# Kernel tuning notes

Hardware: AMD Instinct MI355X
Metric: run time of the kernel (lower is better)

The kernel has to match this reference:

```python
import jax, jax.numpy as jnp
import numpy as np

B = 128
E, IN, H, OUT, ZD = 6, 1664, 512, 618, 32


def setup_inputs() -> dict:
    key = jax.random.key(0)
    ks = jax.random.split(key, 9)
    scale = 0.05
    return {
        "p_prev": jax.random.normal(ks[0], (B, IN), dtype=jnp.float32),
        "blending_coef": jax.random.uniform(ks[1], (B, E), dtype=jnp.float32),
        "z": jax.random.normal(ks[2], (B, ZD), dtype=jnp.float32),
        "w_l1": jax.random.normal(ks[3], (E, IN, H), dtype=jnp.float32) * scale,
        "b_l1": jax.random.normal(ks[4], (E, H), dtype=jnp.float32) * scale,
        "w_l2": jax.random.normal(ks[5], (E, H + ZD, H), dtype=jnp.float32) * scale,
        "b_l2": jax.random.normal(ks[6], (E, H + ZD, H)[0:0] + (E, H), dtype=jnp.float32) * scale,
        "w_l3": jax.random.normal(ks[7], (E, H + ZD, OUT), dtype=jnp.float32) * scale,
        "b_l3": jax.random.normal(ks[8], (E, OUT), dtype=jnp.float32) * scale,
    }


def _moe_layer(x, coef, w, b, use_act=True):
    # Per-sample blended weight matmul, fused as a single contraction:
    # y[b,o] = sum_i x[b,i] * (sum_e coef[b,e] * w[e,i,o]) + sum_e coef[b,e] * b[e,o]
    y = jnp.einsum("bi,eio,be->bo", x, w, coef) + jnp.einsum("be,eo->bo", coef, b)
    return jax.nn.elu(y) if use_act else y


def reference(p_prev, blending_coef, z, w_l1, b_l1, w_l2, b_l2, w_l3, b_l3):
    x = _moe_layer(p_prev, blending_coef, w_l1, b_l1)              # [B, H]
    x = _moe_layer(jnp.concatenate([x, z], axis=-1), blending_coef, w_l2, b_l2)  # [B, H]
    x = _moe_layer(jnp.concatenate([x, z], axis=-1), blending_coef, w_l3, b_l3, use_act=False)  # [B, OUT]
    return x
```

## Files before the change

### kernel.cpp

```cpp
#include <hip/hip_runtime.h>
#include <math.h>

#define B 128
#define E 6
#define IN_DIM 1664
#define H_DIM 512
#define OUT_DIM 618
#define ZD 32
#define K2 544

typedef __attribute__((ext_vector_type(8))) short short8;
typedef __attribute__((ext_vector_type(4))) float f32x4;
union U128 { uint4 u4; short8 s8; ushort us[8]; };

__device__ __forceinline__ ushort f2bf(float f) {
    uint u = __float_as_uint(f);
    u += 0x7fffu + ((u >> 16) & 1u);
    return (ushort)(u >> 16);
}
__device__ __forceinline__ uint pk2(float a, float b) {
    return (uint)f2bf(a) | ((uint)f2bf(b) << 16);
}
__device__ __forceinline__ float elu1(float x) { return x < 0.f ? expm1f(x) : x; }


__global__ __launch_bounds__(256) void init_y1(
    const float* __restrict__ coef, const float* __restrict__ b1,
    float* __restrict__ y1)
{
    const int t = blockIdx.x * 256 + threadIdx.x;
    const int b = t >> 7, o = (t & 127) << 2;
    float4 v = {0.f, 0.f, 0.f, 0.f};
    #pragma unroll
    for (int e = 0; e < E; ++e) {
        const float c = coef[b * E + e];
        const float4 bb = *reinterpret_cast<const float4*>(b1 + e * H_DIM + o);
        v.x = fmaf(c, bb.x, v.x); v.y = fmaf(c, bb.y, v.y);
        v.z = fmaf(c, bb.z, v.z); v.w = fmaf(c, bb.w, v.w);
    }
    *reinterpret_cast<float4*>(y1 + b * H_DIM + o) = v;
}

__global__ __launch_bounds__(256) void gemm1(
    const float* __restrict__ x,
    const float* __restrict__ coef,
    const float* __restrict__ w,
    const float* __restrict__ b2, const float* __restrict__ b3,
    float* __restrict__ y1, float* __restrict__ y2, float* __restrict__ out)
{
    __shared__ ushort bs[24][64][8];
    const int tid = threadIdx.x;

    if (blockIdx.y == 0) {
        const int t = blockIdx.x * 256 + tid;
        {
            const int b = t >> 7, o = (t & 127) << 2;
            float4 v = {0.f, 0.f, 0.f, 0.f};
            #pragma unroll
            for (int e = 0; e < E; ++e) {
                const float c = coef[b * E + e];
                const float4 bb = *reinterpret_cast<const float4*>(b2 + e * H_DIM + o);
                v.x = fmaf(c, bb.x, v.x); v.y = fmaf(c, bb.y, v.y);
                v.z = fmaf(c, bb.z, v.z); v.w = fmaf(c, bb.w, v.w);
            }
            *reinterpret_cast<float4*>(y2 + b * H_DIM + o) = v;
        }
        for (int i = t; i < B * OUT_DIM; i += 64 * 256) {
            const int b = i / OUT_DIM, o = i - b * OUT_DIM;
            float v = 0.f;
            #pragma unroll
            for (int e = 0; e < E; ++e)
                v = fmaf(coef[b * E + e], b3[e * OUT_DIM + o], v);
            out[i] = v;
        }
        return;
    }

    const int kb0 = (blockIdx.y - 1) * 4;
    const int n0 = (blockIdx.x & 31) * 16, rowbase = (blockIdx.x >> 5) * 64;
    const int l = tid & 63, wv = tid >> 6;
    const int tn = tid & 15, tq = tid >> 4;
    const int lp = ((tq >> 2) << 4) | tn, j0 = (2 * tq) & 7;
    const int row = rowbase + wv * 16 + (l & 15);
    const int kq = l >> 4;

    float ce[E];
    #pragma unroll
    for (int e = 0; e < E; ++e) ce[e] = coef[row * E + e];

    float xv[4][8];
    #pragma unroll
    for (int kbi = 0; kbi < 4; ++kbi) {
        const float* p = x + (size_t)row * IN_DIM + (kb0 + kbi) * 32 + kq * 8;
        const float4 a = *reinterpret_cast<const float4*>(p);
        const float4 b = *reinterpret_cast<const float4*>(p + 4);
        xv[kbi][0] = a.x; xv[kbi][1] = a.y; xv[kbi][2] = a.z; xv[kbi][3] = a.w;
        xv[kbi][4] = b.x; xv[kbi][5] = b.y; xv[kbi][6] = b.z; xv[kbi][7] = b.w;
    }

    #pragma unroll
    for (int bb = 0; bb < 2; ++bb) {
        float wr[12][2];
        #pragma unroll
        for (int ss = 0; ss < 12; ++ss) {
            const int s = bb * 12 + ss;
            const int e = s % E, kb = kb0 + s / E;
            const float* src = w + ((size_t)e * IN_DIM + kb * 32 + 2 * tq) * H_DIM + n0 + tn;
            wr[ss][0] = src[0];
            wr[ss][1] = src[H_DIM];
        }
        #pragma unroll
        for (int ss = 0; ss < 12; ++ss)
            *reinterpret_cast<uint*>(&bs[bb * 12 + ss][lp][j0]) =
                pk2(wr[ss][0], wr[ss][1]);
    }
    __syncthreads();

    f32x4 acc = {0.f, 0.f, 0.f, 0.f};
    #pragma unroll
    for (int s = 0; s < 24; ++s) {
        const int e = s % E, kbi = s / E;
        U128 a, b0;
        #pragma unroll
        for (int j = 0; j < 8; ++j) a.us[j] = f2bf(xv[kbi][j] * ce[e]);
        b0.u4 = *reinterpret_cast<const uint4*>(&bs[s][l][0]);
        acc = __builtin_amdgcn_mfma_f32_16x16x32_bf16(a.s8, b0.s8, acc, 0, 0, 0);
    }

    const int colB = n0 + (l & 15);
    const int rowE = rowbase + wv * 16 + ((l >> 4) << 2);
    #pragma unroll
    for (int r = 0; r < 4; ++r)
        atomicAdd(&y1[(size_t)(rowE + r) * H_DIM + colB], acc[r]);
}

template<int KPB, bool ZS, int NW, bool GUARD>
__device__ __forceinline__ void gemm_mid_body(
    const float* __restrict__ yin,
    const float* __restrict__ coef,
    const float* __restrict__ z,
    const float* __restrict__ w,
    float* __restrict__ yout,
    int n0, int rowbase, int kb0, ushort (*bs)[64][8])
{
    constexpr int NS = E * KPB;
    const int tid = threadIdx.x;
    const int l = tid & 63, wv = tid >> 6;
    const int tn = tid & 15, tq = tid >> 4;
    const int lp = ((tq >> 2) << 4) | tn, j0 = (2 * tq) & 7;
    const int row = rowbase + wv * 16 + (l & 15);
    const int kq = l >> 4;
    const bool okS = !GUARD || (n0 + tn) < NW;

    float wr[NS][2];
    #pragma unroll
    for (int s = 0; s < NS; ++s) {
        const int e = s % E, kb = kb0 + s / E;
        const float* src = w + ((size_t)e * K2 + kb * 32 + 2 * tq) * NW + n0 + tn;
        wr[s][0] = okS ? src[0] : 0.f;
        wr[s][1] = okS ? src[NW] : 0.f;
    }

    float ce[E];
    #pragma unroll
    for (int e = 0; e < E; ++e) ce[e] = coef[row * E + e];

    float v[KPB * 8];
    if (ZS) {
        const float4 a = *reinterpret_cast<const float4*>(z + row * ZD + kq * 8);
        const float4 b = *reinterpret_cast<const float4*>(z + row * ZD + kq * 8 + 4);
        v[0] = a.x; v[1] = a.y; v[2] = a.z; v[3] = a.w;
        v[4] = b.x; v[5] = b.y; v[6] = b.z; v[7] = b.w;
    } else {
        #pragma unroll
        for (int kbi = 0; kbi < KPB; ++kbi) {
            const float* p = yin + (size_t)row * H_DIM + (kb0 + kbi) * 32 + kq * 8;
            const float4 a = *reinterpret_cast<const float4*>(p);
            const float4 b = *reinterpret_cast<const float4*>(p + 4);
            v[kbi*8+0] = elu1(a.x); v[kbi*8+1] = elu1(a.y);
            v[kbi*8+2] = elu1(a.z); v[kbi*8+3] = elu1(a.w);
            v[kbi*8+4] = elu1(b.x); v[kbi*8+5] = elu1(b.y);
            v[kbi*8+6] = elu1(b.z); v[kbi*8+7] = elu1(b.w);
        }
    }

    #pragma unroll
    for (int s = 0; s < NS; ++s)
        *reinterpret_cast<uint*>(&bs[s][lp][j0]) = pk2(wr[s][0], wr[s][1]);
    __syncthreads();

    f32x4 acc = {0.f, 0.f, 0.f, 0.f};
    #pragma unroll
    for (int s = 0; s < NS; ++s) {
        const int e = s % E, kbi = s / E;
        U128 a, b0;
        #pragma unroll
        for (int j = 0; j < 8; ++j) a.us[j] = f2bf(v[kbi * 8 + j] * ce[e]);
        b0.u4 = *reinterpret_cast<const uint4*>(&bs[s][l][0]);
        acc = __builtin_amdgcn_mfma_f32_16x16x32_bf16(a.s8, b0.s8, acc, 0, 0, 0);
    }

    const int colB = n0 + (l & 15);
    const int rowE = rowbase + wv * 16 + ((l >> 4) << 2);
    if (!GUARD || colB < NW) {
        #pragma unroll
        for (int r = 0; r < 4; ++r)
            atomicAdd(&yout[(size_t)(rowE + r) * NW + colB], acc[r]);
    }
}

__global__ __launch_bounds__(256) void gemm_l2(
    const float* __restrict__ y1, const float* __restrict__ coef,
    const float* __restrict__ z, const float* __restrict__ w2,
    float* __restrict__ y2)
{
    __shared__ ushort bs[12][64][8];
    const int n0 = (blockIdx.x & 31) * 16, rowbase = (blockIdx.x >> 5) * 64;
    const int sp = blockIdx.y;
    if (sp < 8)
        gemm_mid_body<2, false, H_DIM, false>(y1, coef, z, w2, y2,
                                              n0, rowbase, sp * 2, bs);
    else
        gemm_mid_body<1, true, H_DIM, false>(y1, coef, z, w2, y2,
                                             n0, rowbase, 16, bs);
}

__global__ __launch_bounds__(256) void gemm_l3(
    const float* __restrict__ y2, const float* __restrict__ coef,
    const float* __restrict__ z, const float* __restrict__ w3,
    float* __restrict__ out)
{
    __shared__ ushort bs[12][64][8];
    const int nt = blockIdx.x % 40, rt = blockIdx.x / 40;
    const int n0 = nt * 16, rowbase = rt * 64;
    const int sp = blockIdx.y;
    if (sp < 8)
        gemm_mid_body<2, false, OUT_DIM, true>(y2, coef, z, w3, out,
                                               n0, rowbase, sp * 2, bs);
    else
        gemm_mid_body<1, true, OUT_DIM, true>(y2, coef, z, w3, out,
                                              n0, rowbase, 16, bs);
}

extern "C" void kernel_launch(void* const* d_in, const int* in_sizes, int n_in,
                              void* d_out, int out_size, void* d_ws, size_t ws_size,
                              hipStream_t stream)
{
    const float* p_prev = (const float*)d_in[0];
    const float* coef   = (const float*)d_in[1];
    const float* z      = (const float*)d_in[2];
    const float* w1     = (const float*)d_in[3];
    const float* b1     = (const float*)d_in[4];
    const float* w2     = (const float*)d_in[5];
    const float* b2     = (const float*)d_in[6];
    const float* w3     = (const float*)d_in[7];
    const float* b3     = (const float*)d_in[8];
    float* out = (float*)d_out;

    float* y1 = (float*)d_ws;
    float* y2 = y1 + (size_t)B * H_DIM;

    init_y1<<<64, 256, 0, stream>>>(coef, b1, y1);
    gemm1<<<dim3(64, 14), 256, 0, stream>>>(p_prev, coef, w1, b2, b3,
                                            y1, y2, out);
    gemm_l2<<<dim3(64, 9), 256, 0, stream>>>(y1, coef, z, w2, y2);
    gemm_l3<<<dim3(80, 9), 256, 0, stream>>>(y2, coef, z, w3, out);
}
```

Before: 41.46 us.

## Apply blending coefficients after MFMA via per-expert accumulators

Instead of scaling the activation row by each expert coefficient and converting to bf16 before every MFMA, activations are converted to bf16 once and reused for all experts. Six separate accumulators are kept per expert, and the coefficients are applied in fp32 in the epilogue before the atomic add. The bf16 conversion also switches to the HIP intrinsic. This removes many per-step multiply and convert instructions from the MFMA loop, at the cost of more accumulator registers and a slightly different rounding order.

Result: slower. 43.98 us (+6.1%).

```diff
diff --git a/kernel.cpp b/kernel.cpp
--- a/kernel.cpp
+++ b/kernel.cpp
@@ -1,4 +1,5 @@
 #include <hip/hip_runtime.h>
+#include <hip/hip_bf16.h>
 #include <math.h>
 
 #define B 128
@@ -13,13 +14,11 @@
 typedef __attribute__((ext_vector_type(4))) float f32x4;
 union U128 { uint4 u4; short8 s8; ushort us[8]; };
 
-__device__ __forceinline__ ushort f2bf(float f) {
-    uint u = __float_as_uint(f);
-    u += 0x7fffu + ((u >> 16) & 1u);
-    return (ushort)(u >> 16);
-}
 __device__ __forceinline__ uint pk2(float a, float b) {
-    return (uint)f2bf(a) | ((uint)f2bf(b) << 16);
+    union { __hip_bfloat162 h2; uint u; } cv;
+    cv.h2.x = __float2bfloat16(a);
+    cv.h2.y = __float2bfloat16(b);
+    return cv.u;
 }
 __device__ __forceinline__ float elu1(float x) { return x < 0.f ? expm1f(x) : x; }
 
@@ -81,21 +80,26 @@
     const int l = tid & 63, wv = tid >> 6;
     const int tn = tid & 15, tq = tid >> 4;
     const int lp = ((tq >> 2) << 4) | tn, j0 = (2 * tq) & 7;
-    const int row = rowbase + wv * 16 + (l & 15);
+    const int rowA = rowbase + wv * 16 + (l & 15);
+    const int rowE = rowbase + wv * 16 + ((l >> 4) << 2);
     const int kq = l >> 4;
 
-    float ce[E];
-    #pragma unroll
-    for (int e = 0; e < E; ++e) ce[e] = coef[row * E + e];
-
-    float xv[4][8];
+    float cf[4][E];
+    #pragma unroll
+    for (int r = 0; r < 4; ++r)
+        #pragma unroll
+        for (int e = 0; e < E; ++e)
+            cf[r][e] = coef[(rowE + r) * E + e];
+
+    U128 ax[4];
     #pragma unroll
     for (int kbi = 0; kbi < 4; ++kbi) {
-        const float* p = x + (size_t)row * IN_DIM + (kb0 + kbi) * 32 + kq * 8;
+        const float* p = x + (size_t)rowA * IN_DIM + (kb0 + kbi) * 32 + kq * 8;
         const float4 a = *reinterpret_cast<const float4*>(p);
         const float4 b = *reinterpret_cast<const float4*>(p + 4);
-        xv[kbi][0] = a.x; xv[kbi][1] = a.y; xv[kbi][2] = a.z; xv[kbi][3] = a.w;
-        xv[kbi][4] = b.x; xv[kbi][5] = b.y; xv[kbi][6] = b.z; xv[kbi][7] = b.w;
+        uint* au = reinterpret_cast<uint*>(&ax[kbi]);
+        au[0] = pk2(a.x, a.y); au[1] = pk2(a.z, a.w);
+        au[2] = pk2(b.x, b.y); au[3] = pk2(b.z, b.w);
     }
 
     #pragma unroll
@@ -116,22 +120,26 @@
     }
     __syncthreads();
 
-    f32x4 acc = {0.f, 0.f, 0.f, 0.f};
+    f32x4 acc[E];
+    #pragma unroll
+    for (int e = 0; e < E; ++e) acc[e] = {0.f, 0.f, 0.f, 0.f};
     #pragma unroll
     for (int s = 0; s < 24; ++s) {
         const int e = s % E, kbi = s / E;
-        U128 a, b0;
-        #pragma unroll
-        for (int j = 0; j < 8; ++j) a.us[j] = f2bf(xv[kbi][j] * ce[e]);
+        U128 b0;
         b0.u4 = *reinterpret_cast<const uint4*>(&bs[s][l][0]);
-        acc = __builtin_amdgcn_mfma_f32_16x16x32_bf16(a.s8, b0.s8, acc, 0, 0, 0);
+        acc[e] = __builtin_amdgcn_mfma_f32_16x16x32_bf16(ax[kbi].s8, b0.s8,
+                                                         acc[e], 0, 0, 0);
     }
 
     const int colB = n0 + (l & 15);
-    const int rowE = rowbase + wv * 16 + ((l >> 4) << 2);
-    #pragma unroll
-    for (int r = 0; r < 4; ++r)
-        atomicAdd(&y1[(size_t)(rowE + r) * H_DIM + colB], acc[r]);
+    #pragma unroll
+    for (int r = 0; r < 4; ++r) {
+        float val = 0.f;
+        #pragma unroll
+        for (int e = 0; e < E; ++e) val = fmaf(cf[r][e], acc[e][r], val);
+        atomicAdd(&y1[(size_t)(rowE + r) * H_DIM + colB], val);
+    }
 }
 
 template<int KPB, bool ZS, int NW, bool GUARD>
@@ -148,7 +156,8 @@
     const int l = tid & 63, wv = tid >> 6;
     const int tn = tid & 15, tq = tid >> 4;
     const int lp = ((tq >> 2) << 4) | tn, j0 = (2 * tq) & 7;
-    const int row = rowbase + wv * 16 + (l & 15);
+    const int rowA = rowbase + wv * 16 + (l & 15);
+    const int rowE = rowbase + wv * 16 + ((l >> 4) << 2);
     const int kq = l >> 4;
     const bool okS = !GUARD || (n0 + tn) < NW;
 
@@ -161,26 +170,30 @@
         wr[s][1] = okS ? src[NW] : 0.f;
     }
 
-    float ce[E];
-    #pragma unroll
-    for (int e = 0; e < E; ++e) ce[e] = coef[row * E + e];
-
-    float v[KPB * 8];
+    float cf[4][E];
+    #pragma unroll
+    for (int r = 0; r < 4; ++r)
+        #pragma unroll
+        for (int e = 0; e < E; ++e)
+            cf[r][e] = coef[(rowE + r) * E + e];
+
+    U128 ax[KPB];
     if (ZS) {
-        const float4 a = *reinterpret_cast<const float4*>(z + row * ZD + kq * 8);
-        const float4 b = *reinterpret_cast<const float4*>(z + row * ZD + kq * 8 + 4);
-        v[0] = a.x; v[1] = a.y; v[2] = a.z; v[3] = a.w;
-        v[4] = b.x; v[5] = b.y; v[6] = b.z; v[7] = b.w;
+        const float* p = z + rowA * ZD + kq * 8;
+        const float4 a = *reinterpret_cast<const float4*>(p);
+        const float4 b = *reinterpret_cast<const float4*>(p + 4);
+        uint* au = reinterpret_cast<uint*>(&ax[0]);
+        au[0] = pk2(a.x, a.y); au[1] = pk2(a.z, a.w);
+        au[2] = pk2(b.x, b.y); au[3] = pk2(b.z, b.w);
     } else {
         #pragma unroll
         for (int kbi = 0; kbi < KPB; ++kbi) {
-            const float* p = yin + (size_t)row * H_DIM + (kb0 + kbi) * 32 + kq * 8;
+            const float* p = yin + (size_t)rowA * H_DIM + (kb0 + kbi) * 32 + kq * 8;
             const float4 a = *reinterpret_cast<const float4*>(p);
             const float4 b = *reinterpret_cast<const float4*>(p + 4);
-            v[kbi*8+0] = elu1(a.x); v[kbi*8+1] = elu1(a.y);
-            v[kbi*8+2] = elu1(a.z); v[kbi*8+3] = elu1(a.w);
-            v[kbi*8+4] = elu1(b.x); v[kbi*8+5] = elu1(b.y);
-            v[kbi*8+6] = elu1(b.z); v[kbi*8+7] = elu1(b.w);
+            uint* au = reinterpret_cast<uint*>(&ax[kbi]);
+            au[0] = pk2(elu1(a.x), elu1(a.y)); au[1] = pk2(elu1(a.z), elu1(a.w));
+            au[2] = pk2(elu1(b.x), elu1(b.y)); au[3] = pk2(elu1(b.z), elu1(b.w));
         }
     }
 
@@ -189,23 +202,27 @@
         *reinterpret_cast<uint*>(&bs[s][lp][j0]) = pk2(wr[s][0], wr[s][1]);
     __syncthreads();
 
-    f32x4 acc = {0.f, 0.f, 0.f, 0.f};
+    f32x4 acc[E];
+    #pragma unroll
+    for (int e = 0; e < E; ++e) acc[e] = {0.f, 0.f, 0.f, 0.f};
     #pragma unroll
     for (int s = 0; s < NS; ++s) {
         const int e = s % E, kbi = s / E;
-        U128 a, b0;
-        #pragma unroll
-        for (int j = 0; j < 8; ++j) a.us[j] = f2bf(v[kbi * 8 + j] * ce[e]);
+        U128 b0;
         b0.u4 = *reinterpret_cast<const uint4*>(&bs[s][l][0]);
-        acc = __builtin_amdgcn_mfma_f32_16x16x32_bf16(a.s8, b0.s8, acc, 0, 0, 0);
+        acc[e] = __builtin_amdgcn_mfma_f32_16x16x32_bf16(ax[kbi].s8, b0.s8,
+                                                         acc[e], 0, 0, 0);
     }
 
     const int colB = n0 + (l & 15);
-    const int rowE = rowbase + wv * 16 + ((l >> 4) << 2);
     if (!GUARD || colB < NW) {
         #pragma unroll
-        for (int r = 0; r < 4; ++r)
-            atomicAdd(&yout[(size_t)(rowE + r) * NW + colB], acc[r]);
+        for (int r = 0; r < 4; ++r) {
+            float val = 0.f;
+            #pragma unroll
+            for (int e = 0; e < E; ++e) val = fmaf(cf[r][e], acc[e][r], val);
+            atomicAdd(&yout[(size_t)(rowE + r) * NW + colB], val);
+        }
     }
 }
 
```
